# Kernel optimization log

Hardware: AMD Instinct MI355X
Metric: run time of the kernel (lower is better)

Reference implementation:

```python
import jax, jax.numpy as jnp
import numpy as np

B, S, D, H, HD = 2, 2048, 1024, 16, 64
K, L = 1024, 4  # num_codes, vq_levels


def setup_inputs() -> dict:
    key = jax.random.key(0)
    ks = jax.random.split(key, 12)
    w = lambda k, shape: jax.random.normal(k, shape, jnp.float32) * 0.02
    return {
        "x": jax.random.normal(ks[0], (B, S, D), jnp.float32),
        "ln1_g": jnp.ones((D,), jnp.float32), "ln1_b": jnp.zeros((D,), jnp.float32),
        "wq": w(ks[1], (D, D)), "wk": w(ks[2], (D, D)), "wv": w(ks[3], (D, D)),
        "wg": w(ks[4], (D, D)), "wo": w(ks[5], (D, D)),
        "ln2_g": jnp.ones((D,), jnp.float32), "ln2_b": jnp.zeros((D,), jnp.float32),
        "w1": w(ks[6], (D, 4 * D)), "b1": jnp.zeros((4 * D,), jnp.float32),
        "w2": w(ks[7], (4 * D, D)), "b2": jnp.zeros((D,), jnp.float32),
        "ln3_g": jnp.ones((D,), jnp.float32), "ln3_b": jnp.zeros((D,), jnp.float32),
        "codebooks": jax.random.uniform(ks[8], (L, K, D), jnp.float32, -1.0 / K, 1.0 / K),
    }


def _ln(x, g, b):
    m = jnp.mean(x, -1, keepdims=True)
    v = jnp.var(x, -1, keepdims=True)
    return (x - m) / jnp.sqrt(v + 1e-5) * g + b


def _rope(x):  # x: [B, S, H, HD]
    hd = x.shape[-1]
    inv = 1.0 / (10000.0 ** (jnp.arange(0, hd, 2, dtype=jnp.float32) / hd))
    t = jnp.arange(x.shape[1], dtype=jnp.float32)
    f = jnp.einsum('i,j->ij', t, inv)               # [S, HD/2]
    emb = jnp.concatenate([f, f], -1)               # [S, HD]
    cos = jnp.cos(emb)[None, :, None, :]
    sin = jnp.sin(emb)[None, :, None, :]
    x1, x2 = jnp.split(x, 2, -1)
    rot = jnp.concatenate([-x2, x1], -1)
    return x * cos + rot * sin


def reference(x, ln1_g, ln1_b, wq, wk, wv, wg, wo, ln2_g, ln2_b,
              w1, b1, w2, b2, ln3_g, ln3_b, codebooks):
    # --- retention sub-block (pre-LN) ---
    h = _ln(x, ln1_g, ln1_b)
    q = (h @ wq).reshape(B, S, H, HD)
    k = (h @ wk).reshape(B, S, H, HD)
    v = (h @ wv).reshape(B, S, H, HD)
    q, k = _rope(q), _rope(k)
    q, k, v = (a.transpose(0, 2, 1, 3) for a in (q, k, v))  # [B,H,S,HD]
    i = jnp.arange(S)
    dmask = jnp.tril(i[:, None] - i[None, :]).astype(jnp.float32)  # [S,S], >=0
    gamma = (1.0 - jnp.exp2(-5.0 - jnp.arange(H, dtype=jnp.float32)))[:, None, None]
    decay = (gamma ** dmask) * jnp.tril(jnp.ones((S, S), jnp.float32))  # [H,S,S]
    ret = jnp.einsum('bhqd,bhkd->bhqk', q, k) / np.sqrt(HD).astype(np.float32) * decay
    o = jnp.einsum('bhqk,bhkd->bhqd', ret, v).transpose(0, 2, 1, 3).reshape(B, S, D)
    g = jax.nn.silu(h @ wg)
    x = x + (o * g) @ wo
    # --- MLP sub-block (pre-LN) ---
    h2 = _ln(x, ln2_g, ln2_b)
    x = x + (jax.nn.gelu(h2 @ w1 + b1, approximate=False) @ w2 + b2)
    # --- residual vector quantizer ---
    xn = _ln(x, ln3_g, ln3_b)
    residual, total = xn, jnp.zeros_like(xn)
    ql, el = 0.0, 0.0
    for lvl in range(L):
        cb = codebooks[lvl]                         # [K, D]
        flat = residual.reshape(-1, D)              # [B*S, D]
        d2 = (jnp.sum(flat ** 2, 1, keepdims=True)
              + jnp.sum(cb ** 2, 1) - 2.0 * flat @ cb.T)
        idx = jnp.argmin(d2, 1)
        quant = cb[idx].reshape(xn.shape)
        ql = ql + jnp.mean((quant - jax.lax.stop_gradient(residual)) ** 2)
        el = el + jnp.mean((jax.lax.stop_gradient(quant) - residual) ** 2)
        total = total + quant
        residual = residual - jax.lax.stop_gradient(quant)
    final = xn + jax.lax.stop_gradient(total - xn)  # straight-through
    return (x + final, ql / L, el / L)
```

## Files before the change

### kernel.cpp

```cpp
#include <hip/hip_runtime.h>
#include <cstdint>
#include <cstddef>

#define DEV __device__ __forceinline__

typedef __attribute__((ext_vector_type(8))) short bf16x8;
typedef __attribute__((ext_vector_type(4))) float f32x4;

typedef const __attribute__((address_space(1))) void gl_void;
typedef __attribute__((address_space(3))) void lds_void;

DEV unsigned short f2bf(float f){
  union { float f; uint32_t u; } v; v.f = f;
  uint32_t r = v.u + 0x7FFFu + ((v.u >> 16) & 1u);
  return (unsigned short)(r >> 16);
}
DEV float bf2f(unsigned short u){
  union { uint32_t u; float f; } v; v.u = ((uint32_t)u) << 16; return v.f;
}
DEV uint32_t packbf2(float a, float b){
  return (uint32_t)f2bf(a) | ((uint32_t)f2bf(b) << 16);
}

__global__ void ln_kernel(const float* __restrict__ x, const float* __restrict__ gw,
                          const float* __restrict__ bw, unsigned short* __restrict__ obf,
                          float* __restrict__ of32)
{
  const int row = blockIdx.x, t = threadIdx.x;
  const float4 v = ((const float4*)(x + (size_t)row*1024))[t];
  float s  = v.x + v.y + v.z + v.w;
  float s2 = v.x*v.x + v.y*v.y + v.z*v.z + v.w*v.w;
  #pragma unroll
  for (int o = 32; o >= 1; o >>= 1){ s += __shfl_down(s, o); s2 += __shfl_down(s2, o); }
  __shared__ float red[8];
  const int w = t >> 6, ln = t & 63;
  if (ln == 0){ red[w] = s; red[4+w] = s2; }
  __syncthreads();
  const float fs  = red[0]+red[1]+red[2]+red[3];
  const float fs2 = red[4]+red[5]+red[6]+red[7];
  const float mean = fs * (1.0f/1024.0f);
  const float var  = fs2 * (1.0f/1024.0f) - mean*mean;
  const float rstd = rsqrtf(var + 1e-5f);
  const float4 gv = ((const float4*)gw)[t];
  const float4 bv = ((const float4*)bw)[t];
  float4 o4;
  o4.x = (v.x-mean)*rstd*gv.x + bv.x;
  o4.y = (v.y-mean)*rstd*gv.y + bv.y;
  o4.z = (v.z-mean)*rstd*gv.z + bv.z;
  o4.w = (v.w-mean)*rstd*gv.w + bv.w;
  if (of32) ((float4*)(of32 + (size_t)row*1024))[t] = o4;
  ushort4 ob; ob.x = f2bf(o4.x); ob.y = f2bf(o4.y); ob.z = f2bf(o4.z); ob.w = f2bf(o4.w);
  ((ushort4*)(obf + (size_t)row*1024))[t] = ob;
}

struct Ptr5 { const float* p[5]; };
__global__ void transpose_cvt5(Ptr5 in, unsigned short* __restrict__ out)
{
  __shared__ float tile[32][33];
  const float* src = in.p[blockIdx.z];
  unsigned short* dst = out + (size_t)blockIdx.z*1048576;
  const int c0 = blockIdx.x*32, r0 = blockIdx.y*32;
  const int tx = threadIdx.x & 31, ty = threadIdx.x >> 5;
  #pragma unroll
  for (int i = 0; i < 32; i += 8)
    tile[ty+i][tx] = src[(size_t)(r0+ty+i)*1024 + c0 + tx];
  __syncthreads();
  #pragma unroll
  for (int i = 0; i < 32; i += 8)
    dst[(size_t)(c0+ty+i)*1024 + r0 + tx] = f2bf(tile[tx][ty+i]);
}

__global__ void transpose_cvt(const float* __restrict__ in, unsigned short* __restrict__ out,
                              int R, int C)
{
  __shared__ float tile[32][33];
  const int c0 = blockIdx.x*32, r0 = blockIdx.y*32;
  const int tx = threadIdx.x & 31, ty = threadIdx.x >> 5;
  #pragma unroll
  for (int i = 0; i < 32; i += 8)
    tile[ty+i][tx] = in[(size_t)(r0+ty+i)*C + c0 + tx];
  __syncthreads();
  #pragma unroll
  for (int i = 0; i < 32; i += 8)
    out[(size_t)(c0+ty+i)*R + r0 + tx] = f2bf(tile[tx][ty+i]);
}

__global__ void cvtnorm_kernel(const float* __restrict__ cb, unsigned short* __restrict__ cbbf,
                               float* __restrict__ cbn2)
{
  const int code = blockIdx.x, t = threadIdx.x;
  const float4 v = ((const float4*)(cb + (size_t)code*1024))[t];
  ushort4 o; o.x = f2bf(v.x); o.y = f2bf(v.y); o.z = f2bf(v.z); o.w = f2bf(v.w);
  ((ushort4*)(cbbf + (size_t)code*1024))[t] = o;
  float s = v.x*v.x + v.y*v.y + v.z*v.z + v.w*v.w;
  #pragma unroll
  for (int off = 32; off >= 1; off >>= 1) s += __shfl_down(s, off);
  __shared__ float red[4];
  if ((t & 63) == 0) red[t >> 6] = s;
  __syncthreads();
  if (t == 0) cbn2[code] = red[0]+red[1]+red[2]+red[3];
}

template<int EPI, bool BIAS, bool RES, bool OUTBF>
__global__ __launch_bounds__(256, 4) void gemm_bt(
    const unsigned short* __restrict__ A, const unsigned short* __restrict__ BT,
    void* __restrict__ Cv, const float* __restrict__ bias, const float* __restrict__ resid,
    int M, int N, int K)
{
  __shared__ __align__(16) unsigned short As[2][128*32];
  __shared__ __align__(16) unsigned short Bs[2][128*32];
  const int t = threadIdx.x;
  const int w = t >> 6, ln = t & 63, lg = ln >> 4, lc = ln & 15;
  const int gx = gridDim.x, nwg = gridDim.x * gridDim.y;
  int lin = blockIdx.y * gx + blockIdx.x;
  lin = (lin >> 3) + (lin & 7) * (nwg >> 3);
  const int m0 = (lin / gx) * 128, n0 = (lin % gx) * 128;
  const int wr = (w >> 1) * 64, wc = (w & 1) * 64;
  f32x4 acc[4][4] = {};
  const int nkt = K >> 5;

  auto stage = [&](int buf, int kt){
    #pragma unroll
    for (int c = 0; c < 2; ++c){
      const int chunk = c*256 + t;
      const int row = chunk >> 2, ke = (chunk & 3) * 8;
      __builtin_amdgcn_global_load_lds(
          (gl_void*)(A + (size_t)(m0+row)*K + (size_t)kt*32 + ke),
          (lds_void*)&As[buf][(c*256 + w*64)*8], 16, 0, 0);
      __builtin_amdgcn_global_load_lds(
          (gl_void*)(BT + (size_t)(n0+row)*K + (size_t)kt*32 + ke),
          (lds_void*)&Bs[buf][(c*256 + w*64)*8], 16, 0, 0);
    }
  };

  stage(0, 0);
  __syncthreads();
  for (int kt = 0; kt < nkt; ++kt){
    const int cur = kt & 1;
    if (kt + 1 < nkt) stage(cur ^ 1, kt + 1);
    bf16x8 af[4], bfr[4];
    #pragma unroll
    for (int i = 0; i < 4; ++i){
      af[i]  = *(const bf16x8*)&As[cur][(wr + i*16 + lc)*32 + lg*8];
      bfr[i] = *(const bf16x8*)&Bs[cur][(wc + i*16 + lc)*32 + lg*8];
    }
    #pragma unroll
    for (int m = 0; m < 4; ++m)
      #pragma unroll
      for (int n = 0; n < 4; ++n)
        acc[m][n] = __builtin_amdgcn_mfma_f32_16x16x32_bf16(af[m], bfr[n], acc[m][n], 0, 0, 0);
    __syncthreads();
  }

  if constexpr (EPI == 3){
    const int sect = (n0 + wc) >> 10;
    unsigned short* outp = (unsigned short*)Cv + (size_t)sect*4194304;
    #pragma unroll
    for (int m = 0; m < 4; ++m){
      #pragma unroll
      for (int r = 0; r < 4; ++r){
        const int row = m0 + wr + m*16 + lg*4 + r;
        const int s_ = row & 2047;
        #pragma unroll
        for (int n = 0; n < 4; ++n){
          const int col = n0 + wc + n*16 + lc;
          const int c1 = col & 1023;
          float v = acc[m][n][r];
          if (sect <= 1){
            const int j = c1 & 31;
            const float ang = (float)s_ * exp2f(-(float)j * 0.4152410118609203f);
            float sn, cs; sincosf(ang, &sn, &cs);
            const float vp = acc[m][n ^ 2][r];
            v = (c1 & 32) ? (v*cs + vp*sn) : (v*cs - vp*sn);
          } else if (sect == 3){
            v = v * (1.0f / (1.0f + __expf(-v)));
          }
          outp[(size_t)row*1024 + c1] = f2bf(v);
        }
      }
    }
    return;
  }

  #pragma unroll
  for (int m = 0; m < 4; ++m){
    #pragma unroll
    for (int n = 0; n < 4; ++n){
      #pragma unroll
      for (int r = 0; r < 4; ++r){
        const int row = m0 + wr + m*16 + lg*4 + r;
        const int col = n0 + wc + n*16 + lc;
        float v = acc[m][n][r];
        if constexpr (BIAS) v += bias[col];
        if constexpr (EPI == 1) v = v * (1.0f / (1.0f + __expf(-v)));
        if constexpr (EPI == 2) v = 0.5f * v * (1.0f + erff(v * 0.70710678118654752f));
        if constexpr (RES) v += resid[(size_t)row*N + col];
        if constexpr (OUTBF) ((unsigned short*)Cv)[(size_t)row*N + col] = f2bf(v);
        else                 ((float*)Cv)[(size_t)row*N + col] = v;
      }
    }
  }
}

template<int EPI, bool BIAS, bool RES, bool OUTBF, int NSPLIT>
__global__ __launch_bounds__(256, 3) void gemm64_bt(
    const unsigned short* __restrict__ A, const unsigned short* __restrict__ BT,
    void* __restrict__ Cv, const float* __restrict__ bias, const float* __restrict__ resid,
    int M, int N, int K)
{
  __shared__ __align__(16) unsigned short As[2][64*64];
  __shared__ __align__(16) unsigned short Bs[2][128*64];
  const int t = threadIdx.x;
  const int w = t >> 6, ln = t & 63, lg = ln >> 4, lc = ln & 15;
  const int gx = gridDim.x, nwg = gridDim.x * gridDim.y;
  int lin = blockIdx.y * gx + blockIdx.x;
  lin = (lin >> 3) + (lin & 7) * (nwg >> 3);
  const int bx = lin % gx, by = lin / gx;
  const int m0 = by * 64, n0 = bx * 128;
  const int wr = (w >> 1) * 32, wc = (w & 1) * 64;
  f32x4 acc[2][4] = {};
  const int nkt = (K >> 6) / NSPLIT;
  const int ktb = (NSPLIT > 1) ? blockIdx.z * nkt : 0;

  auto stage = [&](int buf, int kt){
    #pragma unroll
    for (int c = 0; c < 2; ++c){
      const int chunk = c*256 + t;
      const int row = chunk >> 3;
      const int kb = (((chunk & 7) << 4) ^ ((row & 7) << 4)) >> 1;
      __builtin_amdgcn_global_load_lds(
          (gl_void*)(A + (size_t)(m0+row)*K + (size_t)(ktb+kt)*64 + kb),
          (lds_void*)&As[buf][(c*256 + w*64)*8], 16, 0, 0);
    }
    #pragma unroll
    for (int c = 0; c < 4; ++c){
      const int chunk = c*256 + t;
      const int row = chunk >> 3;
      const int kb = (((chunk & 7) << 4) ^ ((row & 7) << 4)) >> 1;
      __builtin_amdgcn_global_load_lds(
          (gl_void*)(BT + (size_t)(n0+row)*K + (size_t)(ktb+kt)*64 + kb),
          (lds_void*)&Bs[buf][(c*256 + w*64)*8], 16, 0, 0);
    }
  };

  stage(0, 0);
  __syncthreads();
  for (int kt = 0; kt < nkt; ++kt){
    const int cur = kt & 1;
    if (kt + 1 < nkt) stage(cur ^ 1, kt + 1);
    #pragma unroll
    for (int ks = 0; ks < 2; ++ks){
      bf16x8 af[2], bfr[4];
      #pragma unroll
      for (int i = 0; i < 2; ++i){
        const int rowA = wr + i*16 + lc;
        const int colA = (((ks<<6) + (lg<<4)) ^ ((rowA & 7) << 4)) >> 1;
        af[i] = *(const bf16x8*)&As[cur][rowA*64 + colA];
      }
      #pragma unroll
      for (int i = 0; i < 4; ++i){
        const int rowB = wc + i*16 + lc;
        const int colB = (((ks<<6) + (lg<<4)) ^ ((rowB & 7) << 4)) >> 1;
        bfr[i] = *(const bf16x8*)&Bs[cur][rowB*64 + colB];
      }
      #pragma unroll
      for (int m = 0; m < 2; ++m)
        #pragma unroll
        for (int n = 0; n < 4; ++n)
          acc[m][n] = __builtin_amdgcn_mfma_f32_16x16x32_bf16(af[m], bfr[n], acc[m][n], 0, 0, 0);
    }
    __syncthreads();
  }

  if constexpr (EPI == 4){
    #pragma unroll
    for (int m = 0; m < 2; ++m){
      #pragma unroll
      for (int r = 0; r < 4; ++r){
        float best = 3.4e38f; int bi = 0;
        #pragma unroll
        for (int n = 0; n < 4; ++n){
          const int col = n0 + wc + n*16 + lc;
          const float d = bias[col] - 2.0f*acc[m][n][r];
          if (d < best){ best = d; bi = col; }
        }
        #pragma unroll
        for (int o = 1; o < 16; o <<= 1){
          const float ob = __shfl_xor(best, o);
          const int oi = __shfl_xor(bi, o);
          if (ob < best || (ob == best && oi < bi)){ best = ob; bi = oi; }
        }
        if (lc == 0){
          const int row = m0 + wr + m*16 + lg*4 + r;
          ((float2*)Cv)[row*16 + bx*2 + (w & 1)] = make_float2(best, (float)bi);
        }
      }
    }
    return;
  }

  float* Cp = (float*)Cv + (NSPLIT > 1 ? (size_t)blockIdx.z * (size_t)M * N : 0);
  #pragma unroll
  for (int m = 0; m < 2; ++m){
    #pragma unroll
    for (int n = 0; n < 4; ++n){
      #pragma unroll
      for (int r = 0; r < 4; ++r){
        const int row = m0 + wr + m*16 + lg*4 + r;
        const int col = n0 + wc + n*16 + lc;
        float v = acc[m][n][r];
        if constexpr (BIAS) v += bias[col];
        if constexpr (RES) v += resid[(size_t)row*N + col];
        if constexpr (OUTBF) ((unsigned short*)Cv)[(size_t)row*N + col] = f2bf(v);
        else                 Cp[(size_t)row*N + col] = v;
      }
    }
  }
}

__global__ void splitk_reduce(const float* __restrict__ p, const float* __restrict__ bias,
                              const float* __restrict__ resid, float* __restrict__ out)
{
  const int i = blockIdx.x*256 + threadIdx.x;
  const float4 a = ((const float4*)p)[i];
  const float4 b = ((const float4*)(p + 4194304))[i];
  const float4 rv = ((const float4*)resid)[i];
  const float4 bv = ((const float4*)bias)[i & 255];
  float4 o;
  o.x = a.x + b.x + rv.x + bv.x;
  o.y = a.y + b.y + rv.y + bv.y;
  o.z = a.z + b.z + rv.z + bv.z;
  o.w = a.w + b.w + rv.w + bv.w;
  ((float4*)out)[i] = o;
}

__global__ __launch_bounds__(256, 2) void chunk_sum(
    const unsigned short* __restrict__ kb, const unsigned short* __restrict__ vb,
    float* __restrict__ Tbuf)
{
  __shared__ unsigned short KT[64*72];
  __shared__ unsigned short VT[64*72];
  const int t = threadIdx.x, w = t >> 6, ln = t & 63, lg = ln >> 4, lc = ln & 15;
  const int blk = blockIdx.x;
  const int bh = blk >> 5, c = blk & 31;
  const int b = bh >> 4, hh = bh & 15;
  const float lg2g = log2f(1.0f - exp2f(-5.0f - (float)hh));
  #pragma unroll
  for (int ch = 0; ch < 2; ++ch){
    const int chunk = ch*256 + t;
    const int i = chunk >> 3, d0 = (chunk & 7)*8;
    const size_t gofs = ((size_t)(b*2048 + c*64 + i))*1024 + hh*64 + d0;
    const float wi = exp2f(lg2g * (float)(64 - i));
    union {uint4 u; unsigned short s[8];} kv, vv;
    kv.u = *(const uint4*)(kb + gofs);
    vv.u = *(const uint4*)(vb + gofs);
    #pragma unroll
    for (int j = 0; j < 8; ++j){
      KT[(d0+j)*72 + i] = f2bf(bf2f(kv.s[j]) * wi);
      VT[(d0+j)*72 + i] = vv.s[j];
    }
  }
  __syncthreads();
  f32x4 acc[4] = {};
  #pragma unroll
  for (int ks = 0; ks < 2; ++ks){
    const bf16x8 af = *(const bf16x8*)&KT[(w*16 + lc)*72 + ks*32 + lg*8];
    #pragma unroll
    for (int n = 0; n < 4; ++n){
      const bf16x8 bf = *(const bf16x8*)&VT[(n*16 + lc)*72 + ks*32 + lg*8];
      acc[n] = __builtin_amdgcn_mfma_f32_16x16x32_bf16(af, bf, acc[n], 0, 0, 0);
    }
  }
  float* out = Tbuf + (size_t)blk*4096;
  #pragma unroll
  for (int n = 0; n < 4; ++n)
    #pragma unroll
    for (int r = 0; r < 4; ++r)
      out[(w*16 + lg*4 + r)*64 + n*16 + lc] = acc[n][r];
}

__global__ void chunk_scan(const float* __restrict__ Tbuf, unsigned short* __restrict__ statesT)
{
  const int bh = blockIdx.x, t = threadIdx.x;
  const int hh = bh & 15;
  const float gamma = 1.0f - exp2f(-5.0f - (float)hh);
  const float g64 = exp2f(log2f(gamma) * 64.0f);
  float S[16];
  #pragma unroll
  for (int j = 0; j < 16; ++j) S[j] = 0.f;
  const int dv = t >> 2, d0 = (t & 3) * 16;
  for (int c = 0; c < 32; ++c){
    const size_t base = ((size_t)(bh*32 + c))*4096;
    union { unsigned short s[8]; uint4 u; } p0, p1;
    #pragma unroll
    for (int j = 0; j < 8; ++j){ p0.s[j] = f2bf(S[j]); p1.s[j] = f2bf(S[8+j]); }
    *(uint4*)(statesT + base + t*16)     = p0.u;
    *(uint4*)(statesT + base + t*16 + 8) = p1.u;
    #pragma unroll
    for (int j = 0; j < 16; ++j)
      S[j] = g64*S[j] + Tbuf[base + (size_t)(d0 + j)*64 + dv];
  }
}

__global__ __launch_bounds__(256, 2) void retention_chunk(
    const unsigned short* __restrict__ qb, const unsigned short* __restrict__ kb,
    const unsigned short* __restrict__ vb, const unsigned short* __restrict__ gb,
    const unsigned short* __restrict__ statesT, unsigned short* __restrict__ og)
{
  __shared__ unsigned short VT[64*72];
  __shared__ unsigned short Pw[64*72];
  const int t = threadIdx.x, w = t >> 6, ln = t & 63, lg = ln >> 4, lc = ln & 15;
  const int blk = blockIdx.x;
  const int bh = blk >> 5, c = blk & 31;
  const int b = bh >> 4, hh = bh & 15;
  const float lg2g = log2f(1.0f - exp2f(-5.0f - (float)hh));
  float gpr[4];
  #pragma unroll
  for (int r = 0; r < 4; ++r) gpr[r] = exp2f(-lg2g * (float)r);
  const size_t rowbase = (size_t)(b*2048 + c*64);

  #pragma unroll
  for (int ch = 0; ch < 2; ++ch){
    const int chunk = ch*256 + t;
    const int i = chunk >> 3, d0 = (chunk & 7)*8;
    union {uint4 u; unsigned short s[8];} vv;
    vv.u = *(const uint4*)(vb + (rowbase + i)*1024 + hh*64 + d0);
    #pragma unroll
    for (int j = 0; j < 8; ++j) VT[(d0+j)*72 + i] = vv.s[j];
  }

  bf16x8 Qf[2], Kf[4][2];
  #pragma unroll
  for (int ks = 0; ks < 2; ++ks){
    union {uint4 u; bf16x8 f;} cv;
    cv.u = *(const uint4*)(qb + (rowbase + w*16 + lc)*1024 + hh*64 + ks*32 + lg*8);
    Qf[ks] = cv.f;
    #pragma unroll
    for (int mt = 0; mt < 4; ++mt){
      union {uint4 u; bf16x8 f;} kv;
      kv.u = *(const uint4*)(kb + (rowbase + mt*16 + lc)*1024 + hh*64 + ks*32 + lg*8);
      Kf[mt][ks] = kv.f;
    }
  }

  f32x4 st[4] = {};
  #pragma unroll
  for (int ks = 0; ks < 2; ++ks)
    #pragma unroll
    for (int mt = 0; mt < 4; ++mt)
      st[mt] = __builtin_amdgcn_mfma_f32_16x16x32_bf16(Kf[mt][ks], Qf[ks], st[mt], 0, 0, 0);

  __syncthreads();

  #pragma unroll
  for (int mt = 0; mt < 4; ++mt){
    const int kp = mt*16 + lg*4;
    const int qrow = w*16 + lc;
    const int delta0 = qrow - kp;
    const float dec0 = exp2f(lg2g * (float)delta0) * 0.125f;
    float vals[4];
    #pragma unroll
    for (int r = 0; r < 4; ++r)
      vals[r] = (delta0 >= r) ? st[mt][r] * dec0 * gpr[r] : 0.0f;
    uint2 pk; pk.x = packbf2(vals[0], vals[1]); pk.y = packbf2(vals[2], vals[3]);
    *(uint2*)&Pw[qrow*72 + kp] = pk;
  }

  f32x4 acc[4] = {};
  const unsigned short* Sbase = statesT + (size_t)blk*4096;
  #pragma unroll
  for (int ks = 0; ks < 2; ++ks)
    #pragma unroll
    for (int n = 0; n < 4; ++n){
      union {uint4 u; bf16x8 f;} sv;
      sv.u = *(const uint4*)(Sbase + (n*16 + lc)*64 + ks*32 + lg*8);
      acc[n] = __builtin_amdgcn_mfma_f32_16x16x32_bf16(Qf[ks], sv.f, acc[n], 0, 0, 0);
    }
  #pragma unroll
  for (int n = 0; n < 4; ++n)
    #pragma unroll
    for (int r = 0; r < 4; ++r)
      acc[n][r] *= exp2f(lg2g * (float)(w*16 + lg*4 + r)) * 0.125f;

  #pragma unroll
  for (int ks = 0; ks < 2; ++ks){
    const bf16x8 Pf = *(const bf16x8*)&Pw[(w*16 + lc)*72 + ks*32 + lg*8];
    #pragma unroll
    for (int n = 0; n < 4; ++n){
      const bf16x8 Vf = *(const bf16x8*)&VT[(n*16 + lc)*72 + ks*32 + lg*8];
      acc[n] = __builtin_amdgcn_mfma_f32_16x16x32_bf16(Pf, Vf, acc[n], 0, 0, 0);
    }
  }

  #pragma unroll
  for (int n = 0; n < 4; ++n){
    #pragma unroll
    for (int r = 0; r < 4; ++r){
      const size_t row = rowbase + w*16 + lg*4 + r;
      const int col = hh*64 + n*16 + lc;
      const float gv = bf2f(gb[row*1024 + col]);
      og[row*1024 + col] = f2bf(acc[n][r] * gv);
    }
  }
}

__global__ void rvq_update3(const float* __restrict__ cb_l, const float2* __restrict__ partials,
                            const float* __restrict__ res_in, float* __restrict__ res_out,
                            unsigned short* __restrict__ resb, float* __restrict__ qlpart, int lvl)
{
  const int m = blockIdx.x, t = threadIdx.x;
  __shared__ int sid;
  if (t == 0){
    float best = 3.4e38f; int bi = 0;
    #pragma unroll
    for (int p = 0; p < 16; ++p){
      const float2 pr = partials[m*16 + p];
      if (pr.x < best){ best = pr.x; bi = (int)pr.y; }
    }
    sid = bi;
  }
  __syncthreads();
  const int id = sid;
  const float4 qv = ((const float4*)(cb_l + (size_t)id*1024))[t];
  const float4 rv = ((const float4*)(res_in + (size_t)m*1024))[t];
  float4 nr; nr.x = rv.x - qv.x; nr.y = rv.y - qv.y; nr.z = rv.z - qv.z; nr.w = rv.w - qv.w;
  ((float4*)(res_out + (size_t)m*1024))[t] = nr;
  ushort4 nb; nb.x = f2bf(nr.x); nb.y = f2bf(nr.y); nb.z = f2bf(nr.z); nb.w = f2bf(nr.w);
  ((ushort4*)(resb + (size_t)m*1024))[t] = nb;
  float s = nr.x*nr.x + nr.y*nr.y + nr.z*nr.z + nr.w*nr.w;
  #pragma unroll
  for (int o = 32; o >= 1; o >>= 1) s += __shfl_down(s, o);
  __shared__ float red[4];
  if ((t & 63) == 0) red[t >> 6] = s;
  __syncthreads();
  if (t == 0) qlpart[lvl*4096 + m] = red[0]+red[1]+red[2]+red[3];
}

__global__ void final_add3(const float* __restrict__ x2, const float* __restrict__ xn,
                           const float* __restrict__ res4, float* __restrict__ out)
{
  const int i = blockIdx.x*256 + threadIdx.x;
  const float4 a = ((const float4*)x2)[i];
  const float4 b = ((const float4*)xn)[i];
  const float4 c = ((const float4*)res4)[i];
  float4 o;
  o.x = a.x + b.x - c.x;
  o.y = a.y + b.y - c.y;
  o.z = a.z + b.z - c.z;
  o.w = a.w + b.w - c.w;
  ((float4*)out)[i] = o;
}

__global__ void ql_final(const float* __restrict__ qlpart, float* __restrict__ outs)
{
  const int t = threadIdx.x;
  float s = 0.f;
  for (int i = t; i < 16384; i += 256) s += qlpart[i];
  #pragma unroll
  for (int o = 32; o >= 1; o >>= 1) s += __shfl_down(s, o);
  __shared__ float red[4];
  if ((t & 63) == 0) red[t >> 6] = s;
  __syncthreads();
  if (t == 0){
    const float q = (red[0]+red[1]+red[2]+red[3]) * (1.0f/4194304.0f) * 0.25f;
    outs[0] = q; outs[1] = q;
  }
}

extern "C" void kernel_launch(void* const* d_in, const int* in_sizes, int n_in,
                              void* d_out, int out_size, void* d_ws, size_t ws_size,
                              hipStream_t stream)
{
  const float* x     = (const float*)d_in[0];
  const float* ln1_g = (const float*)d_in[1];
  const float* ln1_b = (const float*)d_in[2];
  const float* wq    = (const float*)d_in[3];
  const float* wk    = (const float*)d_in[4];
  const float* wv    = (const float*)d_in[5];
  const float* wg    = (const float*)d_in[6];
  const float* wo    = (const float*)d_in[7];
  const float* ln2_g = (const float*)d_in[8];
  const float* ln2_b = (const float*)d_in[9];
  const float* w1    = (const float*)d_in[10];
  const float* b1    = (const float*)d_in[11];
  const float* w2    = (const float*)d_in[12];
  const float* b2    = (const float*)d_in[13];
  const float* ln3_g = (const float*)d_in[14];
  const float* ln3_b = (const float*)d_in[15];
  const float* cb    = (const float*)d_in[16];

  char* ws = (char*)d_ws;
  const size_t MB = 1024*1024;
  unsigned short* wqkvgT = (unsigned short*)(ws + 0*MB);
  unsigned short* w1T  = (unsigned short*)(ws + 10*MB);
  unsigned short* w2T  = (unsigned short*)(ws + 18*MB);
  unsigned short* cbbf = (unsigned short*)(ws + 26*MB);
  float* cbn2     = (float*)(ws + 34*MB);
  float* qlpart   = (float*)(ws + 34*MB + 16*1024);
  float2* partials= (float2*)(ws + 34*MB + 128*1024);
  unsigned short* hbf  = (unsigned short*)(ws + 35*MB);
  unsigned short* qbuf = (unsigned short*)(ws + 43*MB);
  unsigned short* kbuf = (unsigned short*)(ws + 51*MB);
  unsigned short* vbuf = (unsigned short*)(ws + 59*MB);
  unsigned short* gbuf = (unsigned short*)(ws + 67*MB);
  float* skbuf  = (float*)(ws + 43*MB);
  unsigned short* ogb  = (unsigned short*)(ws + 75*MB);
  float* x1     = (float*)(ws + 83*MB);
  unsigned short* h2   = (unsigned short*)(ws + 99*MB);
  unsigned short* a1   = (unsigned short*)(ws + 107*MB);
  float* x2     = (float*)(ws + 139*MB);
  float* Tbuf   = (float*)(ws + 139*MB);
  float* xnf    = (float*)(ws + 155*MB);
  unsigned short* statesT = (unsigned short*)(ws + 155*MB);
  unsigned short* resb = (unsigned short*)(ws + 171*MB);
  float* resw   = (float*)(ws + 187*MB);

  float* outf = (float*)d_out;

  Ptr5 p5; p5.p[0]=wq; p5.p[1]=wk; p5.p[2]=wv; p5.p[3]=wg; p5.p[4]=wo;
  hipLaunchKernelGGL(transpose_cvt5, dim3(32,32,5), dim3(256), 0, stream, p5, wqkvgT);
  hipLaunchKernelGGL(transpose_cvt, dim3(128,32), dim3(256), 0, stream, w1, w1T, 1024, 4096);
  hipLaunchKernelGGL(transpose_cvt, dim3(32,128), dim3(256), 0, stream, w2, w2T, 4096, 1024);
  hipLaunchKernelGGL(cvtnorm_kernel, dim3(4096), dim3(256), 0, stream, cb, cbbf, cbn2);

  hipLaunchKernelGGL(ln_kernel, dim3(4096), dim3(256), 0, stream, x, ln1_g, ln1_b, hbf, (float*)nullptr);
  hipLaunchKernelGGL((gemm_bt<3,false,false,true>), dim3(32,32), dim3(256), 0, stream,
                     hbf, wqkvgT, (void*)qbuf, (const float*)nullptr, (const float*)nullptr, 4096, 4096, 1024);
  hipLaunchKernelGGL(chunk_sum,  dim3(1024), dim3(256), 0, stream, kbuf, vbuf, Tbuf);
  hipLaunchKernelGGL(chunk_scan, dim3(32),   dim3(256), 0, stream, Tbuf, statesT);
  hipLaunchKernelGGL(retention_chunk, dim3(1024), dim3(256), 0, stream,
                     qbuf, kbuf, vbuf, gbuf, statesT, ogb);
  hipLaunchKernelGGL((gemm64_bt<0,false,true,false,1>), dim3(8,64), dim3(256), 0, stream,
                     ogb, wqkvgT + 4194304, (void*)x1, (const float*)nullptr, x, 4096, 1024, 1024);

  hipLaunchKernelGGL(ln_kernel, dim3(4096), dim3(256), 0, stream, x1, ln2_g, ln2_b, h2, (float*)nullptr);
  hipLaunchKernelGGL((gemm_bt<2,true,false,true>), dim3(32,32), dim3(256), 0, stream,
                     h2, w1T, (void*)a1, b1, (const float*)nullptr, 4096, 4096, 1024);
  hipLaunchKernelGGL((gemm64_bt<0,false,false,false,2>), dim3(8,64,2), dim3(256), 0, stream,
                     a1, w2T, (void*)skbuf, (const float*)nullptr, (const float*)nullptr, 4096, 1024, 4096);
  hipLaunchKernelGGL(splitk_reduce, dim3(4096), dim3(256), 0, stream, skbuf, b2, x1, x2);

  hipLaunchKernelGGL(ln_kernel, dim3(4096), dim3(256), 0, stream, x2, ln3_g, ln3_b, resb, xnf);
  for (int lvl = 0; lvl < 4; ++lvl){
    hipLaunchKernelGGL((gemm64_bt<4,false,false,false,1>), dim3(8,64), dim3(256), 0, stream,
                       resb, cbbf + (size_t)lvl*1048576, (void*)partials,
                       cbn2 + lvl*1024, (const float*)nullptr, 4096, 1024, 1024);
    hipLaunchKernelGGL(rvq_update3, dim3(4096), dim3(256), 0, stream,
                       cb + (size_t)lvl*1048576, partials,
                       (lvl == 0) ? xnf : resw, resw, resb, qlpart, lvl);
  }

  hipLaunchKernelGGL(final_add3, dim3(4096), dim3(256), 0, stream, x2, xnf, resw, outf);
  hipLaunchKernelGGL(ql_final, dim3(1), dim3(256), 0, stream, qlpart, outf + 4194304);
}
```

Before: 433.0 us.

## Replace 128x128 GEMM with 256x256 8-wave swizzled LDS kernel and RoPE table

The two large 4096x4096x1024 GEMMs (the fused QKVG projection and MLP up-projection) now use a new 256x256-tile kernel with 512 threads, K-step 64 and an XOR-swizzled 64 KB LDS layout. Prefetch of the next tile is interleaved in halves between four MFMA phases, with s_setprio raised around the MFMA blocks. The larger tile is meant to cut global and LDS traffic per flop and reduce bank conflicts. The RoPE sin/cos is now read from a table built once by a new kernel instead of being computed per element in the epilogue. In exchange the grid drops to 256 workgroups, which lowers occupancy and could underfill the CUs, and the extra barriers add sync cost.

```diff
diff --git a/kernel.cpp b/kernel.cpp
--- a/kernel.cpp
+++ b/kernel.cpp
@@ -101,77 +101,148 @@
   if (t == 0) cbn2[code] = red[0]+red[1]+red[2]+red[3];
 }
 
-template<int EPI, bool BIAS, bool RES, bool OUTBF>
-__global__ __launch_bounds__(256, 4) void gemm_bt(
+__global__ void rope_tab(float2* __restrict__ rt)
+{
+  const int i = blockIdx.x*256 + threadIdx.x;
+  const int s = i >> 5, j = i & 31;
+  const float ang = (float)s * exp2f(-(float)j * 0.4152410118609203f);
+  float sn, cs; sincosf(ang, &sn, &cs);
+  rt[i] = make_float2(cs, sn);
+}
+
+template<int EPI>
+__global__ __launch_bounds__(512, 2) void gemm256(
     const unsigned short* __restrict__ A, const unsigned short* __restrict__ BT,
-    void* __restrict__ Cv, const float* __restrict__ bias, const float* __restrict__ resid,
-    int M, int N, int K)
-{
-  __shared__ __align__(16) unsigned short As[2][128*32];
-  __shared__ __align__(16) unsigned short Bs[2][128*32];
+    unsigned short* __restrict__ C, const float* __restrict__ bias,
+    const float2* __restrict__ rt, int M, int N, int K)
+{
+  __shared__ __align__(16) unsigned short SH[65536];
   const int t = threadIdx.x;
   const int w = t >> 6, ln = t & 63, lg = ln >> 4, lc = ln & 15;
+  const int wm = w >> 2, wn = w & 3;
   const int gx = gridDim.x, nwg = gridDim.x * gridDim.y;
   int lin = blockIdx.y * gx + blockIdx.x;
   lin = (lin >> 3) + (lin & 7) * (nwg >> 3);
-  const int m0 = (lin / gx) * 128, n0 = (lin % gx) * 128;
-  const int wr = (w >> 1) * 64, wc = (w & 1) * 64;
-  f32x4 acc[4][4] = {};
-  const int nkt = K >> 5;
-
-  auto stage = [&](int buf, int kt){
-    #pragma unroll
-    for (int c = 0; c < 2; ++c){
-      const int chunk = c*256 + t;
-      const int row = chunk >> 2, ke = (chunk & 3) * 8;
+  const int m0 = (lin / gx) * 256, n0 = (lin % gx) * 256;
+  const int nkt = K >> 6;
+
+  f32x4 acc[8][4] = {};
+
+  auto stage = [&](int buf, int kt, int half, int isB){
+    const unsigned short* src = isB ? BT : A;
+    const int mb = isB ? n0 : m0;
+    #pragma unroll
+    for (int j = 0; j < 2; ++j){
+      const int u = j*512 + t;
+      const int ro = u >> 3;
+      const int k16 = (u & 7) ^ (ro & 7);
       __builtin_amdgcn_global_load_lds(
-          (gl_void*)(A + (size_t)(m0+row)*K + (size_t)kt*32 + ke),
-          (lds_void*)&As[buf][(c*256 + w*64)*8], 16, 0, 0);
-      __builtin_amdgcn_global_load_lds(
-          (gl_void*)(BT + (size_t)(n0+row)*K + (size_t)kt*32 + ke),
-          (lds_void*)&Bs[buf][(c*256 + w*64)*8], 16, 0, 0);
+        (gl_void*)(src + (size_t)(mb + half*128 + ro)*K + (size_t)kt*64 + k16*8),
+        (lds_void*)&SH[buf*32768 + isB*16384 + half*8192 + (j*512 + (t & ~63))*8],
+        16, 0, 0);
     }
   };
 
-  stage(0, 0);
-  __syncthreads();
+  auto ldA = [&](int buf, int mf, int ks) -> bf16x8 {
+    const int R = wm*128 + mf*16 + lc;
+    const int ci = (ks*32 + lg*8) ^ ((lc & 7) << 3);
+    return *(const bf16x8*)&SH[buf*32768 + R*64 + ci];
+  };
+  auto ldB = [&](int buf, int nf, int ks) -> bf16x8 {
+    const int R = wn*64 + nf*16 + lc;
+    const int ci = (ks*32 + lg*8) ^ ((lc & 7) << 3);
+    return *(const bf16x8*)&SH[buf*32768 + 16384 + R*64 + ci];
+  };
+
+  stage(0, 0, 0, 0); stage(0, 0, 1, 0); stage(0, 0, 0, 1); stage(0, 0, 1, 1);
+  asm volatile("s_waitcnt vmcnt(0)" ::: "memory");
+  __builtin_amdgcn_s_barrier();
+
+  bf16x8 aF[4][2], bF[2][2];
   for (int kt = 0; kt < nkt; ++kt){
     const int cur = kt & 1;
-    if (kt + 1 < nkt) stage(cur ^ 1, kt + 1);
-    bf16x8 af[4], bfr[4];
-    #pragma unroll
-    for (int i = 0; i < 4; ++i){
-      af[i]  = *(const bf16x8*)&As[cur][(wr + i*16 + lc)*32 + lg*8];
-      bfr[i] = *(const bf16x8*)&Bs[cur][(wc + i*16 + lc)*32 + lg*8];
-    }
-    #pragma unroll
-    for (int m = 0; m < 4; ++m)
-      #pragma unroll
-      for (int n = 0; n < 4; ++n)
-        acc[m][n] = __builtin_amdgcn_mfma_f32_16x16x32_bf16(af[m], bfr[n], acc[m][n], 0, 0, 0);
-    __syncthreads();
-  }
-
+    const bool pf = (kt + 1 < nkt);
+
+    #pragma unroll
+    for (int f = 0; f < 4; ++f){ aF[f][0] = ldA(cur, f, 0); aF[f][1] = ldA(cur, f, 1); }
+    #pragma unroll
+    for (int f = 0; f < 2; ++f){ bF[f][0] = ldB(cur, f, 0); bF[f][1] = ldB(cur, f, 1); }
+    if (pf){ stage(cur^1, kt+1, 0, 0); stage(cur^1, kt+1, 0, 1); }
+    __builtin_amdgcn_s_barrier();
+    __builtin_amdgcn_s_setprio(1);
+    #pragma unroll
+    for (int mf = 0; mf < 4; ++mf)
+      #pragma unroll
+      for (int nf = 0; nf < 2; ++nf){
+        acc[mf][nf] = __builtin_amdgcn_mfma_f32_16x16x32_bf16(aF[mf][0], bF[nf][0], acc[mf][nf], 0, 0, 0);
+        acc[mf][nf] = __builtin_amdgcn_mfma_f32_16x16x32_bf16(aF[mf][1], bF[nf][1], acc[mf][nf], 0, 0, 0);
+      }
+    __builtin_amdgcn_s_setprio(0);
+    __builtin_amdgcn_s_barrier();
+
+    #pragma unroll
+    for (int f = 0; f < 2; ++f){ bF[f][0] = ldB(cur, 2+f, 0); bF[f][1] = ldB(cur, 2+f, 1); }
+    if (pf){ stage(cur^1, kt+1, 1, 1); stage(cur^1, kt+1, 1, 0); }
+    __builtin_amdgcn_s_barrier();
+    __builtin_amdgcn_s_setprio(1);
+    #pragma unroll
+    for (int mf = 0; mf < 4; ++mf)
+      #pragma unroll
+      for (int nf = 0; nf < 2; ++nf){
+        acc[mf][2+nf] = __builtin_amdgcn_mfma_f32_16x16x32_bf16(aF[mf][0], bF[nf][0], acc[mf][2+nf], 0, 0, 0);
+        acc[mf][2+nf] = __builtin_amdgcn_mfma_f32_16x16x32_bf16(aF[mf][1], bF[nf][1], acc[mf][2+nf], 0, 0, 0);
+      }
+    __builtin_amdgcn_s_setprio(0);
+    __builtin_amdgcn_s_barrier();
+
+    #pragma unroll
+    for (int f = 0; f < 4; ++f){ aF[f][0] = ldA(cur, 4+f, 0); aF[f][1] = ldA(cur, 4+f, 1); }
+    __builtin_amdgcn_s_barrier();
+    __builtin_amdgcn_s_setprio(1);
+    #pragma unroll
+    for (int mf = 0; mf < 4; ++mf)
+      #pragma unroll
+      for (int nf = 0; nf < 2; ++nf){
+        acc[4+mf][2+nf] = __builtin_amdgcn_mfma_f32_16x16x32_bf16(aF[mf][0], bF[nf][0], acc[4+mf][2+nf], 0, 0, 0);
+        acc[4+mf][2+nf] = __builtin_amdgcn_mfma_f32_16x16x32_bf16(aF[mf][1], bF[nf][1], acc[4+mf][2+nf], 0, 0, 0);
+      }
+    __builtin_amdgcn_s_setprio(0);
+    __builtin_amdgcn_s_barrier();
+
+    #pragma unroll
+    for (int f = 0; f < 2; ++f){ bF[f][0] = ldB(cur, f, 0); bF[f][1] = ldB(cur, f, 1); }
+    __builtin_amdgcn_s_barrier();
+    __builtin_amdgcn_s_setprio(1);
+    #pragma unroll
+    for (int mf = 0; mf < 4; ++mf)
+      #pragma unroll
+      for (int nf = 0; nf < 2; ++nf){
+        acc[4+mf][nf] = __builtin_amdgcn_mfma_f32_16x16x32_bf16(aF[mf][0], bF[nf][0], acc[4+mf][nf], 0, 0, 0);
+        acc[4+mf][nf] = __builtin_amdgcn_mfma_f32_16x16x32_bf16(aF[mf][1], bF[nf][1], acc[4+mf][nf], 0, 0, 0);
+      }
+    __builtin_amdgcn_s_setprio(0);
+    asm volatile("s_waitcnt vmcnt(0)" ::: "memory");
+    __builtin_amdgcn_s_barrier();
+  }
+
+  const int mrow = m0 + wm*128, ncol = n0 + wn*64;
   if constexpr (EPI == 3){
-    const int sect = (n0 + wc) >> 10;
-    unsigned short* outp = (unsigned short*)Cv + (size_t)sect*4194304;
-    #pragma unroll
-    for (int m = 0; m < 4; ++m){
+    const int sect = ncol >> 10;
+    unsigned short* outp = C + (size_t)sect*4194304;
+    #pragma unroll
+    for (int mf = 0; mf < 8; ++mf){
       #pragma unroll
       for (int r = 0; r < 4; ++r){
-        const int row = m0 + wr + m*16 + lg*4 + r;
+        const int row = mrow + mf*16 + lg*4 + r;
         const int s_ = row & 2047;
         #pragma unroll
-        for (int n = 0; n < 4; ++n){
-          const int col = n0 + wc + n*16 + lc;
-          const int c1 = col & 1023;
-          float v = acc[m][n][r];
+        for (int nf = 0; nf < 4; ++nf){
+          const int c1 = (ncol + nf*16 + lc) & 1023;
+          float v = acc[mf][nf][r];
           if (sect <= 1){
-            const int j = c1 & 31;
-            const float ang = (float)s_ * exp2f(-(float)j * 0.4152410118609203f);
-            float sn, cs; sincosf(ang, &sn, &cs);
-            const float vp = acc[m][n ^ 2][r];
-            v = (c1 & 32) ? (v*cs + vp*sn) : (v*cs - vp*sn);
+            const float2 cs = rt[(s_ << 5) + (c1 & 31)];
+            const float vp = acc[mf][nf ^ 2][r];
+            v = (c1 & 32) ? (v*cs.x + vp*cs.y) : (v*cs.x - vp*cs.y);
           } else if (sect == 3){
             v = v * (1.0f / (1.0f + __expf(-v)));
           }
@@ -179,24 +250,19 @@
         }
       }
     }
-    return;
-  }
-
-  #pragma unroll
-  for (int m = 0; m < 4; ++m){
-    #pragma unroll
-    for (int n = 0; n < 4; ++n){
+  } else {
+    #pragma unroll
+    for (int mf = 0; mf < 8; ++mf){
       #pragma unroll
       for (int r = 0; r < 4; ++r){
-        const int row = m0 + wr + m*16 + lg*4 + r;
-        const int col = n0 + wc + n*16 + lc;
-        float v = acc[m][n][r];
-        if constexpr (BIAS) v += bias[col];
-        if constexpr (EPI == 1) v = v * (1.0f / (1.0f + __expf(-v)));
-        if constexpr (EPI == 2) v = 0.5f * v * (1.0f + erff(v * 0.70710678118654752f));
-        if constexpr (RES) v += resid[(size_t)row*N + col];
-        if constexpr (OUTBF) ((unsigned short*)Cv)[(size_t)row*N + col] = f2bf(v);
-        else                 ((float*)Cv)[(size_t)row*N + col] = v;
+        const int row = mrow + mf*16 + lg*4 + r;
+        #pragma unroll
+        for (int nf = 0; nf < 4; ++nf){
+          const int col = ncol + nf*16 + lc;
+          float v = acc[mf][nf][r] + bias[col];
+          v = 0.5f * v * (1.0f + erff(v * 0.70710678118654752f));
+          C[(size_t)row*N + col] = f2bf(v);
+        }
       }
     }
   }
@@ -613,6 +679,7 @@
   float* xnf    = (float*)(ws + 155*MB);
   unsigned short* statesT = (unsigned short*)(ws + 155*MB);
   unsigned short* resb = (unsigned short*)(ws + 171*MB);
+  float2* rtab  = (float2*)(ws + 179*MB);
   float* resw   = (float*)(ws + 187*MB);
 
   float* outf = (float*)d_out;
@@ -622,10 +689,11 @@
   hipLaunchKernelGGL(transpose_cvt, dim3(128,32), dim3(256), 0, stream, w1, w1T, 1024, 4096);
   hipLaunchKernelGGL(transpose_cvt, dim3(32,128), dim3(256), 0, stream, w2, w2T, 4096, 1024);
   hipLaunchKernelGGL(cvtnorm_kernel, dim3(4096), dim3(256), 0, stream, cb, cbbf, cbn2);
+  hipLaunchKernelGGL(rope_tab, dim3(256), dim3(256), 0, stream, rtab);
 
   hipLaunchKernelGGL(ln_kernel, dim3(4096), dim3(256), 0, stream, x, ln1_g, ln1_b, hbf, (float*)nullptr);
-  hipLaunchKernelGGL((gemm_bt<3,false,false,true>), dim3(32,32), dim3(256), 0, stream,
-                     hbf, wqkvgT, (void*)qbuf, (const float*)nullptr, (const float*)nullptr, 4096, 4096, 1024);
+  hipLaunchKernelGGL((gemm256<3>), dim3(16,16), dim3(512), 0, stream,
+                     hbf, wqkvgT, qbuf, (const float*)nullptr, (const float2*)rtab, 4096, 4096, 1024);
   hipLaunchKernelGGL(chunk_sum,  dim3(1024), dim3(256), 0, stream, kbuf, vbuf, Tbuf);
   hipLaunchKernelGGL(chunk_scan, dim3(32),   dim3(256), 0, stream, Tbuf, statesT);
   hipLaunchKernelGGL(retention_chunk, dim3(1024), dim3(256), 0, stream,
@@ -634,8 +702,8 @@
                      ogb, wqkvgT + 4194304, (void*)x1, (const float*)nullptr, x, 4096, 1024, 1024);
 
   hipLaunchKernelGGL(ln_kernel, dim3(4096), dim3(256), 0, stream, x1, ln2_g, ln2_b, h2, (float*)nullptr);
-  hipLaunchKernelGGL((gemm_bt<2,true,false,true>), dim3(32,32), dim3(256), 0, stream,
-                     h2, w1T, (void*)a1, b1, (const float*)nullptr, 4096, 4096, 1024);
+  hipLaunchKernelGGL((gemm256<2>), dim3(16,16), dim3(512), 0, stream,
+                     h2, w1T, a1, b1, (const float2*)rtab, 4096, 4096, 1024);
   hipLaunchKernelGGL((gemm64_bt<0,false,false,false,2>), dim3(8,64,2), dim3(256), 0, stream,
                      a1, w2T, (void*)skbuf, (const float*)nullptr, (const float*)nullptr, 4096, 1024, 4096);
   hipLaunchKernelGGL(splitk_reduce, dim3(4096), dim3(256), 0, stream, skbuf, b2, x1, x2);
```

After: 435.9 us. About the same (+0.7%).
